# Kernel optimization log

Measured on AMD Instinct MI355X. Metric: run time of the kernel, lower is better.

## Reference

```python
import jax, jax.numpy as jnp
import numpy as np

NX = 96      # polar grid size (nx x nx)
NETA = 96    # cartesian grid size (neta x neta)
B = 64       # batch


def _rotation_index(n):
    # Static permutation: nx copies of the flat index grid, each rolled by (-i,-i).
    idx = np.arange(n * n).reshape(n, n)
    return np.concatenate([np.roll(idx, shift=(-i, -i), axis=(0, 1)) for i in range(n)], axis=0)  # [n*n, n]


def setup_inputs() -> dict:
    key = jax.random.key(0)
    ks = jax.random.split(key, 18)
    f = lambda k, s: jax.random.normal(k, s, dtype=jnp.float32) * 0.05
    inp = {
        "inputs": f(ks[0], (B, 2, NX * NX)),
        "cart_mat": f(ks[1], (NETA * NETA, NX * NX)),
    }
    for i, name in enumerate(["pre1", "pre2", "pre3", "pre4", "post1", "post2", "post3", "post4"]):
        inp[name] = f(ks[2 + i], (1, NX))
    for i, name in enumerate(["cos_kernel1", "sin_kernel1", "cos_kernel2", "sin_kernel2",
                              "cos_kernel3", "sin_kernel3", "cos_kernel4", "sin_kernel4"]):
        inp[name] = f(ks[10 + i], (NX, NX))
    return inp


def reference(inputs, cart_mat, pre1, pre2, pre3, pre4, post1, post2, post3, post4,
              cos_kernel1, sin_kernel1, cos_kernel2, sin_kernel2,
              cos_kernel3, sin_kernel3, cos_kernel4, sin_kernel4):
    nx, neta = NX, NETA
    ridx = jnp.asarray(_rotation_index(nx).reshape(-1))  # [nx^3] static gather indices
    R, I = inputs[:, 0, :], inputs[:, 1, :]              # each [B, nx^2]
    # Rotation-index gather (vectorized over batch), -> [B*nx, nx, nx]
    Rs = jnp.take(R, ridx, axis=1).reshape(-1, nx, nx)
    Is = jnp.take(I, ridx, axis=1).reshape(-1, nx, nx)

    def helper(pre, post, kernel2, kernel1, data):
        # post @ (kernel2 * ((data * pre) @ kernel1)) : [B*nx, 1, nx]
        return jnp.matmul(post, kernel2 * jnp.matmul(data * pre, kernel1))

    output_polar = (helper(pre1, post1, cos_kernel1, cos_kernel2, Rs)
                    + helper(pre2, post2, sin_kernel1, sin_kernel2, Rs)
                    + helper(pre3, post3, cos_kernel3, sin_kernel3, Is)
                    + helper(pre4, post4, sin_kernel4, cos_kernel4, Is))  # [B*nx, 1, nx]
    output_polar = output_polar.reshape(-1, nx * nx)  # [B, nx^2]
    # Batched polar->cartesian: cart_mat @ x per sample == x @ cart_mat.T
    output_cart = jnp.einsum('bn,mn->bm', output_polar, cart_mat)  # [B, neta^2]
    return output_cart.reshape(-1, neta, neta, 1)
```

## Files before the change

### kernel.cpp

```cpp
#include <hip/hip_runtime.h>

typedef __bf16 bf16x8 __attribute__((ext_vector_type(8)));
typedef float floatx4 __attribute__((ext_vector_type(4)));

__device__ __forceinline__ unsigned short f2bf_bits(float f) {
  __bf16 h = (__bf16)f;
  return __builtin_bit_cast(unsigned short, h);
}

__global__ __launch_bounds__(256) void k_prep(
    const float* __restrict__ pre1, const float* __restrict__ pre2,
    const float* __restrict__ pre3, const float* __restrict__ pre4,
    const float* __restrict__ post1, const float* __restrict__ post2,
    const float* __restrict__ post3, const float* __restrict__ post4,
    const float* __restrict__ ck1, const float* __restrict__ sk1,
    const float* __restrict__ ck2, const float* __restrict__ sk2,
    const float* __restrict__ ck3, const float* __restrict__ sk3,
    const float* __restrict__ ck4, const float* __restrict__ sk4,
    unsigned short* __restrict__ Pt, float* __restrict__ Qt)
{
  int idx = blockIdx.x * 256 + threadIdx.x;
  int h = idx / 9216;
  int rem = idx - h * 9216;
  int c = rem / 96;
  int x = rem - c * 96;
  const float* pre  = (h == 0) ? pre1 : (h == 1) ? pre2 : (h == 2) ? pre3 : pre4;
  const float* post = (h == 0) ? post1 : (h == 1) ? post2 : (h == 2) ? post3 : post4;
  const float* K1   = (h == 0) ? ck2 : (h == 1) ? sk2 : (h == 2) ? sk3 : ck4;
  const float* K2   = (h == 0) ? ck1 : (h == 1) ? sk1 : (h == 2) ? ck3 : sk4;
  Pt[idx] = f2bf_bits(pre[x] * K1[x * 96 + c]);
  Qt[idx] = post[x] * K2[x * 96 + c];
}

__global__ __launch_bounds__(256) void k_stage1(
    const float* __restrict__ inputs,
    const unsigned short* __restrict__ Pt,
    const float* __restrict__ Qt,
    unsigned short* __restrict__ polar)
{
  __shared__ unsigned short Mt[96][104];
  __shared__ float pacc[96];

  int bi = blockIdx.x;
  int b = bi / 96;
  int i = bi - b * 96;
  int tid = threadIdx.x;
  int lane = tid & 63;
  int w = tid >> 6;

  if (tid < 96) pacc[tid] = 0.f;

  const float* srcB = inputs + (size_t)b * 18432;

  int hsel = (w >> 1);
  int l15 = lane & 15;
  int cbase = (w & 1) * 48 + l15;
  int kg = (lane >> 4) * 8;
  int rg = (lane >> 4) * 4;

  for (int ph = 0; ph < 2; ++ph) {
    const float* src = srcB + ph * 9216;
    __syncthreads();
    for (int e = tid; e < 9216; e += 256) {
      int r = e / 96;
      int j = e - r * 96;
      int sr = r + i; if (sr >= 96) sr -= 96;
      int sc = j + i; if (sc >= 96) sc -= 96;
      Mt[r][j] = f2bf_bits(src[sr * 96 + sc]);
    }
    __syncthreads();

    int h = ph * 2 + hsel;
    const unsigned short* PtH = Pt + h * 9216;
    const float* QtH = Qt + h * 9216;

    floatx4 acc[3][6];
    floatx4 zero = {0.f, 0.f, 0.f, 0.f};
#pragma unroll
    for (int ct = 0; ct < 3; ++ct)
#pragma unroll
      for (int rt = 0; rt < 6; ++rt)
        acc[ct][rt] = zero;

#pragma unroll
    for (int ks = 0; ks < 3; ++ks) {
      bf16x8 bfr[3];
#pragma unroll
      for (int ct = 0; ct < 3; ++ct)
        bfr[ct] = *reinterpret_cast<const bf16x8*>(PtH + (cbase + ct * 16) * 96 + ks * 32 + kg);
#pragma unroll
      for (int rt = 0; rt < 6; ++rt) {
        bf16x8 af = *reinterpret_cast<const bf16x8*>(&Mt[rt * 16 + l15][ks * 32 + kg]);
#pragma unroll
        for (int ct = 0; ct < 3; ++ct)
          acc[ct][rt] = __builtin_amdgcn_mfma_f32_16x16x32_bf16(af, bfr[ct], acc[ct][rt], 0, 0, 0);
      }
    }

#pragma unroll
    for (int ct = 0; ct < 3; ++ct) {
      int c = cbase + ct * 16;
      float p = 0.f;
#pragma unroll
      for (int rt = 0; rt < 6; ++rt) {
        floatx4 qv = *reinterpret_cast<const floatx4*>(QtH + c * 96 + rt * 16 + rg);
        p += qv[0] * acc[ct][rt][0] + qv[1] * acc[ct][rt][1]
           + qv[2] * acc[ct][rt][2] + qv[3] * acc[ct][rt][3];
      }
      p += __shfl_xor(p, 16);
      p += __shfl_xor(p, 32);
      if (lane < 16) atomicAdd(&pacc[c], p);
    }
  }

  __syncthreads();
  if (tid < 96) {
    polar[(size_t)b * 9216 + i * 96 + tid] = f2bf_bits(pacc[tid]);
  }
}

__global__ __launch_bounds__(256) void k_stage2(
    const unsigned short* __restrict__ polar,
    const float* __restrict__ cart,
    float* __restrict__ part)
{
  int tid = threadIdx.x;
  int lane = tid & 63;
  int w = tid >> 6;
  int l15 = lane & 15;
  int m = blockIdx.x * 64 + w * 16 + l15;
  int kg = (lane >> 4) * 8;
  int k0 = blockIdx.y * 1152;

  floatx4 acc[4] = {};

  const float* crow = cart + (size_t)m * 9216 + k0 + kg;
  const unsigned short* prow = polar + (size_t)l15 * 9216 + k0 + kg;

  for (int ks = 0; ks < 36; ++ks) {
    floatx4 c0 = *reinterpret_cast<const floatx4*>(crow);
    floatx4 c1 = *reinterpret_cast<const floatx4*>(crow + 4);
    bf16x8 bf;
    bf[0] = (__bf16)c0[0]; bf[1] = (__bf16)c0[1]; bf[2] = (__bf16)c0[2]; bf[3] = (__bf16)c0[3];
    bf[4] = (__bf16)c1[0]; bf[5] = (__bf16)c1[1]; bf[6] = (__bf16)c1[2]; bf[7] = (__bf16)c1[3];
#pragma unroll
    for (int bt = 0; bt < 4; ++bt) {
      bf16x8 af = *reinterpret_cast<const bf16x8*>(prow + bt * 147456);
      acc[bt] = __builtin_amdgcn_mfma_f32_16x16x32_bf16(af, bf, acc[bt], 0, 0, 0);
    }
    crow += 32;
    prow += 32;
  }

  int rg = (lane >> 4) * 4;
#pragma unroll
  for (int bt = 0; bt < 4; ++bt) {
    int b0 = bt * 16 + rg;
#pragma unroll
    for (int q = 0; q < 4; ++q) {
      part[((size_t)blockIdx.y * 64 + b0 + q) * 9216 + m] = acc[bt][q];
    }
  }
}

__global__ __launch_bounds__(256) void k_reduce(
    const float* __restrict__ part, float* __restrict__ out)
{
  int idx = blockIdx.x * 256 + threadIdx.x;
  float s = 0.f;
#pragma unroll
  for (int sp = 0; sp < 8; ++sp) s += part[(size_t)sp * 589824 + idx];
  out[idx] = s;
}

extern "C" void kernel_launch(void* const* d_in, const int* in_sizes, int n_in,
                              void* d_out, int out_size, void* d_ws, size_t ws_size,
                              hipStream_t stream) {
  const float* inputs = (const float*)d_in[0];
  const float* cart   = (const float*)d_in[1];

  char* ws = (char*)d_ws;
  unsigned short* Pt    = (unsigned short*)(ws + 0);
  float*          Qt    = (float*)(ws + 73728);
  unsigned short* polar = (unsigned short*)(ws + 221184);
  float*          part  = (float*)(ws + 1400832);

  k_prep<<<144, 256, 0, stream>>>(
      (const float*)d_in[2],  (const float*)d_in[3],  (const float*)d_in[4],  (const float*)d_in[5],
      (const float*)d_in[6],  (const float*)d_in[7],  (const float*)d_in[8],  (const float*)d_in[9],
      (const float*)d_in[10], (const float*)d_in[11], (const float*)d_in[12], (const float*)d_in[13],
      (const float*)d_in[14], (const float*)d_in[15], (const float*)d_in[16], (const float*)d_in[17],
      Pt, Qt);

  k_stage1<<<6144, 256, 0, stream>>>(inputs, Pt, Qt, polar);

  k_stage2<<<dim3(144, 8), 256, 0, stream>>>(polar, cart, part);

  k_reduce<<<2304, 256, 0, stream>>>(part, (float*)d_out);
}
```

Measured before the change: 711.7 us.

## Move rotation into precomputed weights so input tile loads once per batch

Result: slower. 871.9 us (+22.5%).

```diff
diff --git a/kernel.cpp b/kernel.cpp
--- a/kernel.cpp
+++ b/kernel.cpp
@@ -8,55 +8,67 @@
   return __builtin_bit_cast(unsigned short, h);
 }
 
-__global__ __launch_bounds__(256) void k_prep(
+__global__ __launch_bounds__(256) void k_prep_p(
     const float* __restrict__ pre1, const float* __restrict__ pre2,
     const float* __restrict__ pre3, const float* __restrict__ pre4,
+    const float* __restrict__ ck2, const float* __restrict__ sk2,
+    const float* __restrict__ sk3, const float* __restrict__ ck4,
+    float* __restrict__ Pf)
+{
+  int idx = blockIdx.x * 256 + threadIdx.x;
+  int h = idx / 9216;
+  int rem = idx - h * 9216;
+  int k = rem / 96;
+  const float* pre = (h == 0) ? pre1 : (h == 1) ? pre2 : (h == 2) ? pre3 : pre4;
+  const float* K1  = (h == 0) ? ck2  : (h == 1) ? sk2  : (h == 2) ? sk3  : ck4;
+  Pf[idx] = pre[k] * K1[rem];
+}
+
+__global__ __launch_bounds__(256) void k_prep_q(
     const float* __restrict__ post1, const float* __restrict__ post2,
     const float* __restrict__ post3, const float* __restrict__ post4,
     const float* __restrict__ ck1, const float* __restrict__ sk1,
-    const float* __restrict__ ck2, const float* __restrict__ sk2,
-    const float* __restrict__ ck3, const float* __restrict__ sk3,
-    const float* __restrict__ ck4, const float* __restrict__ sk4,
-    unsigned short* __restrict__ Pt, float* __restrict__ Qt)
+    const float* __restrict__ ck3, const float* __restrict__ sk4,
+    unsigned short* __restrict__ Qrot)
 {
   int idx = blockIdx.x * 256 + threadIdx.x;
-  int h = idx / 9216;
-  int rem = idx - h * 9216;
-  int c = rem / 96;
-  int x = rem - c * 96;
-  const float* pre  = (h == 0) ? pre1 : (h == 1) ? pre2 : (h == 2) ? pre3 : pre4;
+  int i = idx / 36864;
+  int rem = idx - i * 36864;
+  int h = rem / 9216;
+  int rem2 = rem - h * 9216;
+  int c = rem2 / 96;
+  int r = rem2 - c * 96;
+  int rr = r - i; if (rr < 0) rr += 96;
   const float* post = (h == 0) ? post1 : (h == 1) ? post2 : (h == 2) ? post3 : post4;
-  const float* K1   = (h == 0) ? ck2 : (h == 1) ? sk2 : (h == 2) ? sk3 : ck4;
-  const float* K2   = (h == 0) ? ck1 : (h == 1) ? sk1 : (h == 2) ? ck3 : sk4;
-  Pt[idx] = f2bf_bits(pre[x] * K1[x * 96 + c]);
-  Qt[idx] = post[x] * K2[x * 96 + c];
-}
-
-__global__ __launch_bounds__(256) void k_stage1(
+  const float* K2   = (h == 0) ? ck1   : (h == 1) ? sk1   : (h == 2) ? ck3   : sk4;
+  Qrot[idx] = f2bf_bits(post[rr] * K2[rr * 96 + c]);
+}
+
+__global__ __launch_bounds__(256, 4) void k_stage1(
     const float* __restrict__ inputs,
-    const unsigned short* __restrict__ Pt,
-    const float* __restrict__ Qt,
+    const unsigned short* __restrict__ Qrot,
+    const float* __restrict__ Pf,
     unsigned short* __restrict__ polar)
 {
-  __shared__ unsigned short Mt[96][104];
-  __shared__ float pacc[96];
-
-  int bi = blockIdx.x;
-  int b = bi / 96;
-  int i = bi - b * 96;
+  __shared__ unsigned short XdT[96][104];
+  __shared__ float pacc[6][96];
+
+  int blk = blockIdx.x;
+  int b = blk >> 4;
+  int g = blk & 15;
+  int i0 = g * 6;
   int tid = threadIdx.x;
   int lane = tid & 63;
   int w = tid >> 6;
-
-  if (tid < 96) pacc[tid] = 0.f;
+  int l15 = lane & 15;
+  int lg = lane >> 4;
+  int kg = lg * 8;
+  int hsel = w >> 1;
+  int chalf = (w & 1) * 48;
+
+  for (int e = tid; e < 576; e += 256) ((float*)pacc)[e] = 0.f;
 
   const float* srcB = inputs + (size_t)b * 18432;
-
-  int hsel = (w >> 1);
-  int l15 = lane & 15;
-  int cbase = (w & 1) * 48 + l15;
-  int kg = (lane >> 4) * 8;
-  int rg = (lane >> 4) * 4;
 
   for (int ph = 0; ph < 2; ++ph) {
     const float* src = srcB + ph * 9216;
@@ -64,58 +76,82 @@
     for (int e = tid; e < 9216; e += 256) {
       int r = e / 96;
       int j = e - r * 96;
-      int sr = r + i; if (sr >= 96) sr -= 96;
-      int sc = j + i; if (sc >= 96) sc -= 96;
-      Mt[r][j] = f2bf_bits(src[sr * 96 + sc]);
+      XdT[j][r] = f2bf_bits(src[e]);
     }
     __syncthreads();
 
     int h = ph * 2 + hsel;
-    const unsigned short* PtH = Pt + h * 9216;
-    const float* QtH = Qt + h * 9216;
-
-    floatx4 acc[3][6];
-    floatx4 zero = {0.f, 0.f, 0.f, 0.f};
-#pragma unroll
-    for (int ct = 0; ct < 3; ++ct)
-#pragma unroll
-      for (int rt = 0; rt < 6; ++rt)
-        acc[ct][rt] = zero;
-
-#pragma unroll
-    for (int ks = 0; ks < 3; ++ks) {
-      bf16x8 bfr[3];
-#pragma unroll
-      for (int ct = 0; ct < 3; ++ct)
-        bfr[ct] = *reinterpret_cast<const bf16x8*>(PtH + (cbase + ct * 16) * 96 + ks * 32 + kg);
-#pragma unroll
-      for (int rt = 0; rt < 6; ++rt) {
-        bf16x8 af = *reinterpret_cast<const bf16x8*>(&Mt[rt * 16 + l15][ks * 32 + kg]);
+    const unsigned short* QrH = Qrot + h * 9216;
+    const float* PfH = Pf + h * 9216;
+
+    for (int ii = 0; ii < 6; ++ii) {
+      int i = i0 + ii;
+      const unsigned short* QrI = QrH + (size_t)i * 36864;
+      floatx4 svc[3];
+      svc[0] = 0.f; svc[1] = 0.f; svc[2] = 0.f;
+
+#pragma unroll
+      for (int pass = 0; pass < 2; ++pass) {
+        floatx4 acc[3][3];
 #pragma unroll
         for (int ct = 0; ct < 3; ++ct)
-          acc[ct][rt] = __builtin_amdgcn_mfma_f32_16x16x32_bf16(af, bfr[ct], acc[ct][rt], 0, 0, 0);
+#pragma unroll
+          for (int ntl = 0; ntl < 3; ++ntl)
+            acc[ct][ntl] = 0.f;
+
+#pragma unroll
+        for (int ks = 0; ks < 3; ++ks) {
+          bf16x8 afr[3];
+#pragma unroll
+          for (int ct = 0; ct < 3; ++ct)
+            afr[ct] = *reinterpret_cast<const bf16x8*>(
+                QrI + (chalf + ct * 16 + l15) * 96 + ks * 32 + kg);
+#pragma unroll
+          for (int ntl = 0; ntl < 3; ++ntl) {
+            int nt = pass * 3 + ntl;
+            bf16x8 bfr = *reinterpret_cast<const bf16x8*>(
+                &XdT[nt * 16 + l15][ks * 32 + kg]);
+#pragma unroll
+            for (int ct = 0; ct < 3; ++ct)
+              acc[ct][ntl] = __builtin_amdgcn_mfma_f32_16x16x32_bf16(
+                  afr[ct], bfr, acc[ct][ntl], 0, 0, 0);
+          }
+        }
+
+#pragma unroll
+        for (int ct = 0; ct < 3; ++ct) {
+          int c0 = chalf + ct * 16 + lg * 4;
+#pragma unroll
+          for (int ntl = 0; ntl < 3; ++ntl) {
+            int nt = pass * 3 + ntl;
+            int krot = nt * 16 + l15 - i; if (krot < 0) krot += 96;
+            floatx4 pw = *reinterpret_cast<const floatx4*>(PfH + krot * 96 + c0);
+            svc[ct] += pw * acc[ct][ntl];
+          }
+        }
       }
-    }
-
-#pragma unroll
-    for (int ct = 0; ct < 3; ++ct) {
-      int c = cbase + ct * 16;
-      float p = 0.f;
-#pragma unroll
-      for (int rt = 0; rt < 6; ++rt) {
-        floatx4 qv = *reinterpret_cast<const floatx4*>(QtH + c * 96 + rt * 16 + rg);
-        p += qv[0] * acc[ct][rt][0] + qv[1] * acc[ct][rt][1]
-           + qv[2] * acc[ct][rt][2] + qv[3] * acc[ct][rt][3];
+
+#pragma unroll
+      for (int ct = 0; ct < 3; ++ct) {
+        int c0 = chalf + ct * 16 + lg * 4;
+#pragma unroll
+        for (int q = 0; q < 4; ++q) {
+          float v = svc[ct][q];
+          v += __shfl_xor(v, 1);
+          v += __shfl_xor(v, 2);
+          v += __shfl_xor(v, 4);
+          v += __shfl_xor(v, 8);
+          if (l15 == 0) atomicAdd(&pacc[ii][c0 + q], v);
+        }
       }
-      p += __shfl_xor(p, 16);
-      p += __shfl_xor(p, 32);
-      if (lane < 16) atomicAdd(&pacc[c], p);
     }
   }
 
   __syncthreads();
-  if (tid < 96) {
-    polar[(size_t)b * 9216 + i * 96 + tid] = f2bf_bits(pacc[tid]);
+  for (int e = tid; e < 576; e += 256) {
+    int ii = e / 96;
+    int c = e - ii * 96;
+    polar[(size_t)b * 9216 + (i0 + ii) * 96 + c] = f2bf_bits(pacc[ii][c]);
   }
 }
 
@@ -130,14 +166,14 @@
   int l15 = lane & 15;
   int m = blockIdx.x * 64 + w * 16 + l15;
   int kg = (lane >> 4) * 8;
-  int k0 = blockIdx.y * 1152;
+  int k0 = blockIdx.y * 576;
 
   floatx4 acc[4] = {};
 
   const float* crow = cart + (size_t)m * 9216 + k0 + kg;
   const unsigned short* prow = polar + (size_t)l15 * 9216 + k0 + kg;
 
-  for (int ks = 0; ks < 36; ++ks) {
+  for (int ks = 0; ks < 18; ++ks) {
     floatx4 c0 = *reinterpret_cast<const floatx4*>(crow);
     floatx4 c1 = *reinterpret_cast<const floatx4*>(crow + 4);
     bf16x8 bf;
@@ -169,7 +205,7 @@
   int idx = blockIdx.x * 256 + threadIdx.x;
   float s = 0.f;
 #pragma unroll
-  for (int sp = 0; sp < 8; ++sp) s += part[(size_t)sp * 589824 + idx];
+  for (int sp = 0; sp < 16; ++sp) s += part[(size_t)sp * 589824 + idx];
   out[idx] = s;
 }
 
@@ -180,21 +216,24 @@
   const float* cart   = (const float*)d_in[1];
 
   char* ws = (char*)d_ws;
-  unsigned short* Pt    = (unsigned short*)(ws + 0);
-  float*          Qt    = (float*)(ws + 73728);
-  unsigned short* polar = (unsigned short*)(ws + 221184);
-  float*          part  = (float*)(ws + 1400832);
-
-  k_prep<<<144, 256, 0, stream>>>(
+  float*          Pf    = (float*)(ws + 0);
+  unsigned short* Qrot  = (unsigned short*)(ws + 147456);
+  unsigned short* polar = (unsigned short*)(ws + 7225344);
+  float*          part  = (float*)(ws + 8404992);
+
+  k_prep_p<<<144, 256, 0, stream>>>(
       (const float*)d_in[2],  (const float*)d_in[3],  (const float*)d_in[4],  (const float*)d_in[5],
+      (const float*)d_in[12], (const float*)d_in[13], (const float*)d_in[15], (const float*)d_in[16],
+      Pf);
+
+  k_prep_q<<<13824, 256, 0, stream>>>(
       (const float*)d_in[6],  (const float*)d_in[7],  (const float*)d_in[8],  (const float*)d_in[9],
-      (const float*)d_in[10], (const float*)d_in[11], (const float*)d_in[12], (const float*)d_in[13],
-      (const float*)d_in[14], (const float*)d_in[15], (const float*)d_in[16], (const float*)d_in[17],
-      Pt, Qt);
-
-  k_stage1<<<6144, 256, 0, stream>>>(inputs, Pt, Qt, polar);
-
-  k_stage2<<<dim3(144, 8), 256, 0, stream>>>(polar, cart, part);
+      (const float*)d_in[10], (const float*)d_in[11], (const float*)d_in[14], (const float*)d_in[17],
+      Qrot);
+
+  k_stage1<<<1024, 256, 0, stream>>>(inputs, Qrot, Pf, polar);
+
+  k_stage2<<<dim3(144, 16), 256, 0, stream>>>(polar, cart, part);
 
   k_reduce<<<2304, 256, 0, stream>>>(part, (float*)d_out);
 }
```
